# Kernel tuning notes

Measured on AMD Instinct MI355X. Metric: run time of the kernel, lower is better.

## Reference

```python
import jax, jax.numpy as jnp
import numpy as np

B, C, Hs, Ws = 8, 512, 32, 32
NUM_HEADS, D_K = 8, 64
SCALE = D_K ** -0.5


def setup_inputs() -> dict:
    key = jax.random.key(0)
    ks = jax.random.split(key, 8)
    inner = NUM_HEADS * D_K  # 512
    s = 0.02
    return {
        "x": jax.random.normal(ks[0], (B, C, Hs, Ws), dtype=jnp.float32),
        "y": jax.random.normal(ks[1], (B, C, Hs, Ws), dtype=jnp.float32),
        "Wq": jax.random.normal(ks[2], (inner, C), dtype=jnp.float32) * s,
        "bq": jnp.zeros((inner,), dtype=jnp.float32),
        "Wkv": jax.random.normal(ks[3], (2 * inner, C), dtype=jnp.float32) * s,
        "bkv": jnp.zeros((2 * inner,), dtype=jnp.float32),
        "Wp": jax.random.normal(ks[4], (C, inner), dtype=jnp.float32) * s,
        "bp": jnp.zeros((C,), dtype=jnp.float32),
    }


def reference(x, y, Wq, bq, Wkv, bkv, Wp, bp):
    # Faithful to CrossAttentionBlock.forward: y is only shape-checked, unused.
    x_shape = x.shape
    b, c = x.shape[0], x.shape[1]
    # channel_transfer: [B, C, H, W] -> [B, H, W, C] -> [B, N, C]
    xt = jnp.transpose(x, (0, 2, 3, 1)).reshape(b, -1, c)
    n = xt.shape[1]
    # q: [B, N, H*dk] -> [B, H, N, dk]
    q = (xt @ Wq.T + bq).reshape(b, n, NUM_HEADS, D_K).transpose(0, 2, 1, 3)
    # kv: [B, N, 2*H*dk] -> [2, B, H, N, dk]
    kv = (xt @ Wkv.T + bkv).reshape(b, n, 2, NUM_HEADS, D_K).transpose(2, 0, 3, 1, 4)
    k, v = kv[0], kv[1]
    atten = jnp.einsum("bhik,bhjk->bhij", q, k) * SCALE
    atten = jax.nn.softmax(atten, axis=-1)
    res = jnp.einsum("bhij,bhjd->bhid", atten, v)  # [B, H, N, dk]
    res = res.transpose(0, 2, 1, 3).reshape(b, n, NUM_HEADS * D_K)
    res = res @ Wp.T + bp  # [B, N, C]
    # original does a raw reshape of [B, N, C] back into x_shape [B, C, H, W]
    return res.reshape(x_shape)
```

## Files before the change

### kernel.cpp

```cpp
#include <hip/hip_runtime.h>
#include <math.h>

#define BB 8
#define CC 512
#define NH 8
#define DK 64
#define NN 1024
#define MROWS (BB * NN)
#define INNER 512
#define SCALE 0.125f


typedef __attribute__((ext_vector_type(8))) short bf16x8;
typedef __attribute__((ext_vector_type(4))) float floatx4;

__device__ inline short f2bf(float f) {
    union { float f; unsigned u; } un;
    un.f = f;
    unsigned r = un.u + 0x7fffu + ((un.u >> 16) & 1u);
    return (short)(r >> 16);
}

__device__ inline short f2bf_rhu(float f) {
    union { float f; unsigned u; } un;
    un.f = f;
    return (short)((un.u + 0x8000u) >> 16);
}

#define GLD_LDS(gptr, lptr)                                                  \
    __builtin_amdgcn_global_load_lds(                                        \
        (const __attribute__((address_space(1))) void*)(gptr),               \
        (__attribute__((address_space(3))) void*)(lptr), 16, 0, 0)

__global__ __launch_bounds__(256) void prep_kernel(
    const float* __restrict__ x, const float* __restrict__ Wq,
    const float* __restrict__ Wkv, const float* __restrict__ Wp,
    const float* __restrict__ bq, const float* __restrict__ bkv,
    short* __restrict__ xtb, short* __restrict__ wqkvb,
    short* __restrict__ wpb, float* __restrict__ bqkv) {
    __shared__ float tile[32][33];
    const int bid = blockIdx.x;
    if (bid < 4096) {
        const int n0 = (bid & 31) * 32;
        const int c0 = ((bid >> 5) & 15) * 32;
        const int b = bid >> 9;
        const int tx = threadIdx.x & 31;
        const int ty = threadIdx.x >> 5;
        const float* xb = x + (size_t)b * CC * NN;
        short* xo = xtb + (size_t)b * NN * CC;
        for (int i = ty; i < 32; i += 8)
            tile[i][tx] = xb[(size_t)(c0 + i) * NN + n0 + tx];
        __syncthreads();
        for (int i = ty; i < 32; i += 8)
            xo[(size_t)(n0 + i) * CC + c0 + tx] = f2bf(tile[tx][i]);
    } else {
        const int i = (bid - 4096) * 1024 + threadIdx.x * 4;
        if (i < 786432) {
            float4 v = (i < 262144) ? *(const float4*)&Wq[i]
                                    : *(const float4*)&Wkv[i - 262144];
            wqkvb[i + 0] = f2bf(v.x);
            wqkvb[i + 1] = f2bf(v.y);
            wqkvb[i + 2] = f2bf(v.z);
            wqkvb[i + 3] = f2bf(v.w);
        } else if (i < 1048576) {
            const int j = i - 786432;
            float4 v = *(const float4*)&Wp[j];
            wpb[j + 0] = f2bf(v.x);
            wpb[j + 1] = f2bf(v.y);
            wpb[j + 2] = f2bf(v.z);
            wpb[j + 3] = f2bf(v.w);
        } else {
            const int j = i - 1048576;
            if (j < 1536) {
                float4 v = (j < 512) ? *(const float4*)&bq[j]
                                     : *(const float4*)&bkv[j - 512];
                *(float4*)&bqkv[j] = v;
            }
        }
    }
}

template <int MODE, int BN>
__global__ __launch_bounds__(256) void gemm_mfma_kernel(
    const short* __restrict__ A, const short* __restrict__ W,
    const float* __restrict__ bias, float* __restrict__ outf,
    short* __restrict__ outq, short* __restrict__ outk,
    short* __restrict__ outv) {
    constexpr int K = 512;
    constexpr int WCOLS = BN / 64;
    constexpr int WROWS = 4 / WCOLS;
    constexpr int WRSPAN = 128 / WROWS;
    constexpr int RT = WRSPAN / 16;
    constexpr int ABUF = 128 * 32;
    constexpr int BBUF = BN * 32;
    constexpr int STAGE_EL = 2 * ABUF + 2 * BBUF;
    constexpr int CS_EL = (MODE == 1) ? 128 * 132 : 0;
    constexpr int SMEM_EL = (CS_EL > STAGE_EL) ? CS_EL : STAGE_EL;
    __shared__ short smem[SMEM_EL];
    short* As = smem;
    short* Bs = smem + 2 * ABUF;

    const int t = threadIdx.x;
    const int wave = t >> 6;
    const int lane = t & 63;
    const int col = lane & 15;
    const int quad = lane >> 4;
    const int wr = wave / WCOLS;
    const int wc = wave % WCOLS;

    const int bm0 = blockIdx.x * 128;
    const int bn0 = blockIdx.y * BN;

    floatx4 acc[RT][4];
#pragma unroll
    for (int i = 0; i < RT; i++)
#pragma unroll
        for (int j = 0; j < 4; j++) acc[i][j] = (floatx4){0.f, 0.f, 0.f, 0.f};

    const int kpE = (lane & 3) * 8;
    const int rA = wave * 32 + (lane >> 2);
    const short* Ag = A + (size_t)(bm0 + rA) * K + kpE;
    const int rB = wave * (BN / 4) + (lane >> 2);
    const short* Wg = W + (size_t)(bn0 + rB) * K + kpE;
    const int aOff = wave * 1024;
    const int bOff = wave * (BN / 4) * 32;

#define GSTAGE(K0, BUF)                                                       \
    do {                                                                      \
        GLD_LDS(Ag + (K0), As + (BUF)*ABUF + aOff);                           \
        GLD_LDS(Ag + 16 * K + (K0), As + (BUF)*ABUF + aOff + 512);            \
        if constexpr (BN == 128) {                                            \
            GLD_LDS(Wg + (K0), Bs + (BUF)*BBUF + bOff);                       \
            GLD_LDS(Wg + 16 * K + (K0), Bs + (BUF)*BBUF + bOff + 512);        \
        } else {                                                              \
            GLD_LDS(Wg + (K0), Bs + (BUF)*BBUF + bOff);                       \
        }                                                                     \
    } while (0)

    GSTAGE(0, 0);

#pragma unroll
    for (int it = 0; it < 16; it++) {
        const int buf = it & 1;
        __syncthreads();
        if (it < 15) GSTAGE((it + 1) * 32, buf ^ 1);

        const short* A_ = As + buf * ABUF;
        const short* B_ = Bs + buf * BBUF;
        bf16x8 aF[RT], bF[4];
#pragma unroll
        for (int rt = 0; rt < RT; rt++)
            aF[rt] =
                *(const bf16x8*)&A_[(wr * WRSPAN + rt * 16 + col) * 32 + quad * 8];
#pragma unroll
        for (int ct = 0; ct < 4; ct++)
            bF[ct] = *(const bf16x8*)&B_[(wc * 64 + ct * 16 + col) * 32 + quad * 8];
#pragma unroll
        for (int rt = 0; rt < RT; rt++)
#pragma unroll
            for (int ct = 0; ct < 4; ct++)
                acc[rt][ct] = __builtin_amdgcn_mfma_f32_16x16x32_bf16(
                    aF[rt], bF[ct], acc[rt][ct], 0, 0, 0);
    }
#undef GSTAGE

    if (MODE == 1) {
        short* Cs = smem;
        const bool isV = (bn0 >= 1024);
        const bool isQ = (bn0 < 512);
        __syncthreads();
        if (isV) {
#pragma unroll
            for (int rt = 0; rt < RT; rt++) {
#pragma unroll
                for (int ct = 0; ct < 4; ct++) {
                    const int jn_l = wc * 64 + ct * 16 + col;
                    const float bsv = bias[bn0 + jn_l];
                    const int m_l = wr * WRSPAN + rt * 16 + quad * 4;
                    short4 v4;
                    v4.x = f2bf(acc[rt][ct][0] + bsv);
                    v4.y = f2bf(acc[rt][ct][1] + bsv);
                    v4.z = f2bf(acc[rt][ct][2] + bsv);
                    v4.w = f2bf(acc[rt][ct][3] + bsv);
                    *(short4*)&Cs[jn_l * 132 + m_l] = v4;
                }
            }
        } else {
#pragma unroll
            for (int rt = 0; rt < RT; rt++) {
#pragma unroll
                for (int ct = 0; ct < 4; ct++) {
                    const int jn_l = wc * 64 + ct * 16 + col;
                    const float bsv = bias[bn0 + jn_l];
#pragma unroll
                    for (int r = 0; r < 4; r++) {
                        const int m_l = wr * WRSPAN + rt * 16 + quad * 4 + r;
                        const float val = acc[rt][ct][r] + bsv;
                        Cs[m_l * 132 + jn_l] =
                            isQ ? f2bf(val * SCALE) : f2bf(val);
                    }
                }
            }
        }
        __syncthreads();
        const int b = bm0 >> 10;
        const int nbase = bm0 & 1023;
        if (isV) {
#pragma unroll
            for (int p = 0; p < 8; p++) {
                const int cid = p * 256 + t;
                const int jn_l = cid >> 4;
                const int m0 = (cid & 15) * 8;
                bf16x8 frag = *(const bf16x8*)&Cs[jn_l * 132 + m0];
                const int jn_g = bn0 + jn_l;
                const int h = (jn_g >> 6) & 7;
                const int d = jn_g & 63;
                *(bf16x8*)&outv[(((size_t)(b * NH + h)) * DK + d) * NN + nbase +
                                m0] = frag;
            }
        } else {
            short* dst = isQ ? outq : outk;
#pragma unroll
            for (int p = 0; p < 8; p++) {
                const int cid = p * 256 + t;
                const int m_l = cid >> 4;
                const int jn0 = (cid & 15) * 8;
                bf16x8 frag = *(const bf16x8*)&Cs[m_l * 132 + jn0];
                const int jn_g = bn0 + jn0;
                const int h = (jn_g >> 6) & 7;
                const int d = jn_g & 63;
                *(bf16x8*)&dst[(((size_t)(b * NH + h)) * NN + nbase + m_l) * DK +
                               d] = frag;
            }
        }
        return;
    }

#pragma unroll
    for (int rt = 0; rt < RT; rt++) {
#pragma unroll
        for (int ct = 0; ct < 4; ct++) {
            const int jn = bn0 + wc * 64 + ct * 16 + col;
            const float bsv = bias[jn];
#pragma unroll
            for (int r = 0; r < 4; r++) {
                const int m = bm0 + wr * WRSPAN + rt * 16 + quad * 4 + r;
                outf[(size_t)m * 512 + jn] = acc[rt][ct][r] + bsv;
            }
        }
    }
}

__global__ __launch_bounds__(512) void attn_mfma_kernel(
    const short* __restrict__ q, const short* __restrict__ k,
    const short* __restrict__ vt, short* __restrict__ out) {
    const int bh = blockIdx.x;
    const int b = bh >> 3;
    const int h = bh & 7;
    const int n0 = blockIdx.y * 128;
    const int tid = threadIdx.x;
    const int wave = tid >> 6;
    const int lane = tid & 63;
    const int col = lane & 15;
    const int quad = lane >> 4;

    __shared__ short Ks[2][64 * 64];
    __shared__ short Vs[2][64 * 64];
    __shared__ short Ps[8][16][72];

    bf16x8 qa0, qa1;
    {
        const size_t qoff = ((size_t)bh * NN + n0 + wave * 16 + col) * DK;
        qa0 = *(const bf16x8*)&q[qoff + quad * 8];
        qa1 = *(const bf16x8*)&q[qoff + 32 + quad * 8];
    }

    floatx4 o[4];
#pragma unroll
    for (int i = 0; i < 4; i++) o[i] = (floatx4){0.f, 0.f, 0.f, 0.f};
    float l_run[4] = {0.f, 0.f, 0.f, 0.f};

    const short* kg = k + (size_t)bh * NN * DK;
    const short* vg = vt + (size_t)bh * DK * NN;

    const int srow = lane >> 3;
    const int sunit = (lane & 7) ^ srow;
    const int sbase = (wave & 3) * 16;

    const int xs = col & 7;
    const int pK0 = (quad ^ xs) * 8;
    const int pK1 = ((quad + 4) ^ xs) * 8;

#define STAGE(J0, BUF)                                                         \
    do {                                                                       \
        if (wave < 4) {                                                        \
            GLD_LDS(kg + (size_t)((J0) + sbase + srow) * DK + sunit * 8,       \
                    &Ks[BUF][sbase * 64]);                                     \
            GLD_LDS(kg + (size_t)((J0) + sbase + 8 + srow) * DK + sunit * 8,   \
                    &Ks[BUF][(sbase + 8) * 64]);                               \
        } else {                                                               \
            GLD_LDS(vg + (size_t)(sbase + srow) * NN + (J0) + sunit * 8,       \
                    &Vs[BUF][sbase * 64]);                                     \
            GLD_LDS(vg + (size_t)(sbase + 8 + srow) * NN + (J0) + sunit * 8,   \
                    &Vs[BUF][(sbase + 8) * 64]);                               \
        }                                                                      \
    } while (0)

    STAGE(0, 0);

    for (int c = 0; c < 16; c++) {
        const int buf = c & 1;
        __syncthreads();
        if (c < 15) STAGE((c + 1) * 64, buf ^ 1);

        const short* K_ = &Ks[buf][0];
        const short* V_ = &Vs[buf][0];

        float p[4][4];
#pragma unroll
        for (int ct = 0; ct < 4; ct++) {
            bf16x8 kb0 = *(const bf16x8*)&K_[(ct * 16 + col) * 64 + pK0];
            bf16x8 kb1 = *(const bf16x8*)&K_[(ct * 16 + col) * 64 + pK1];
            floatx4 acc = (floatx4){0.f, 0.f, 0.f, 0.f};
            acc = __builtin_amdgcn_mfma_f32_16x16x32_bf16(qa0, kb0, acc, 0, 0, 0);
            acc = __builtin_amdgcn_mfma_f32_16x16x32_bf16(qa1, kb1, acc, 0, 0, 0);
#pragma unroll
            for (int r = 0; r < 4; r++) p[ct][r] = __expf(acc[r]);
        }

#pragma unroll
        for (int r = 0; r < 4; r++)
            l_run[r] += (p[0][r] + p[1][r]) + (p[2][r] + p[3][r]);

#pragma unroll
        for (int ct = 0; ct < 4; ct++)
#pragma unroll
            for (int r = 0; r < 4; r++)
                Ps[wave][quad * 4 + r][ct * 16 + col] = f2bf_rhu(p[ct][r]);

        bf16x8 pa0 = *(const bf16x8*)&Ps[wave][col][quad * 8];
        bf16x8 pa1 = *(const bf16x8*)&Ps[wave][col][32 + quad * 8];

#pragma unroll
        for (int dt = 0; dt < 4; dt++) {
            bf16x8 vb0 = *(const bf16x8*)&V_[(dt * 16 + col) * 64 + pK0];
            bf16x8 vb1 = *(const bf16x8*)&V_[(dt * 16 + col) * 64 + pK1];
            o[dt] = __builtin_amdgcn_mfma_f32_16x16x32_bf16(pa0, vb0, o[dt], 0, 0, 0);
            o[dt] = __builtin_amdgcn_mfma_f32_16x16x32_bf16(pa1, vb1, o[dt], 0, 0, 0);
        }
    }
#undef STAGE

    float inv[4];
#pragma unroll
    for (int r = 0; r < 4; r++) {
        float lv = l_run[r];
#pragma unroll
        for (int d = 1; d < 16; d <<= 1) lv += __shfl_xor(lv, d, 64);
        inv[r] = 1.f / lv;
    }
#pragma unroll
    for (int dt = 0; dt < 4; dt++)
#pragma unroll
        for (int r = 0; r < 4; r++)
            Ps[wave][quad * 4 + r][dt * 16 + col] = f2bf(o[dt][r] * inv[r]);

    {
        const int row = lane >> 2;
        const int d0 = (lane & 3) * 16;
        bf16x8 f0 = *(const bf16x8*)&Ps[wave][row][d0];
        bf16x8 f1 = *(const bf16x8*)&Ps[wave][row][d0 + 8];
        const int m = n0 + wave * 16 + row;
        short* orow = out + ((size_t)(b * NN + m)) * 512 + h * 64 + d0;
        *(bf16x8*)&orow[0] = f0;
        *(bf16x8*)&orow[8] = f1;
    }
}

extern "C" void kernel_launch(void* const* d_in, const int* in_sizes, int n_in,
                              void* d_out, int out_size, void* d_ws,
                              size_t ws_size, hipStream_t stream) {
    const float* x = (const float*)d_in[0];
    const float* Wq = (const float*)d_in[2];
    const float* bq = (const float*)d_in[3];
    const float* Wkv = (const float*)d_in[4];
    const float* bkv = (const float*)d_in[5];
    const float* Wp = (const float*)d_in[6];
    const float* bp = (const float*)d_in[7];
    float* out = (float*)d_out;

    short* ws = (short*)d_ws;
    short* xtb = ws;
    short* qb = xtb + (size_t)MROWS * CC;
    short* kb = qb + (size_t)MROWS * INNER;
    short* vb = kb + (size_t)MROWS * INNER;
    short* wqkvb = vb + (size_t)MROWS * INNER;
    short* wpb = wqkvb + (size_t)3 * INNER * CC;
    float* bqkv = (float*)(wpb + (size_t)CC * INNER);
    short* att = xtb;

    prep_kernel<<<4096 + 1026, 256, 0, stream>>>(x, Wq, Wkv, Wp, bq, bkv, xtb,
                                                 wqkvb, wpb, bqkv);
    {
        dim3 grid(MROWS / 128, (3 * INNER) / 128);
        gemm_mfma_kernel<1, 128><<<grid, 256, 0, stream>>>(
            xtb, wqkvb, bqkv, nullptr, qb, kb, vb);
    }
    {
        dim3 grid(BB * NH, NN / 128);
        attn_mfma_kernel<<<grid, 512, 0, stream>>>(qb, kb, vb, att);
    }
    {
        dim3 grid(MROWS / 128, CC / 64);
        gemm_mfma_kernel<0, 64><<<grid, 256, 0, stream>>>(
            att, wpb, bp, out, nullptr, nullptr, nullptr);
    }
}
```

Baseline: 150.9 us.

## Process two query row tiles per wave in attention kernel, halving block size

Each wave now handles 32 query rows (two 16-row MFMA tiles) instead of 16, so each K and V fragment read from LDS feeds two MFMAs. Blocks shrink from 512 to 256 threads, and every wave stages both K and V. The aim is to halve LDS fragment traffic per unit of MFMA work. In exchange, register pressure per wave roughly doubles for accumulators and probabilities, and each block has fewer waves to hide latency.

```diff
diff --git a/kernel.cpp b/kernel.cpp
--- a/kernel.cpp
+++ b/kernel.cpp
@@ -251,7 +251,7 @@
     }
 }
 
-__global__ __launch_bounds__(512) void attn_mfma_kernel(
+__global__ __launch_bounds__(256) void attn_mfma_kernel(
     const short* __restrict__ q, const short* __restrict__ k,
     const short* __restrict__ vt, short* __restrict__ out) {
     const int bh = blockIdx.x;
@@ -266,26 +266,30 @@
 
     __shared__ short Ks[2][64 * 64];
     __shared__ short Vs[2][64 * 64];
-    __shared__ short Ps[8][16][72];
-
-    bf16x8 qa0, qa1;
-    {
-        const size_t qoff = ((size_t)bh * NN + n0 + wave * 16 + col) * DK;
-        qa0 = *(const bf16x8*)&q[qoff + quad * 8];
-        qa1 = *(const bf16x8*)&q[qoff + 32 + quad * 8];
-    }
-
-    floatx4 o[4];
-#pragma unroll
-    for (int i = 0; i < 4; i++) o[i] = (floatx4){0.f, 0.f, 0.f, 0.f};
-    float l_run[4] = {0.f, 0.f, 0.f, 0.f};
+    __shared__ short Ps[4][32][72];
+
+    bf16x8 qa[2][2];
+#pragma unroll
+    for (int rt = 0; rt < 2; rt++) {
+        const size_t qoff =
+            ((size_t)bh * NN + n0 + wave * 32 + rt * 16 + col) * DK;
+        qa[rt][0] = *(const bf16x8*)&q[qoff + quad * 8];
+        qa[rt][1] = *(const bf16x8*)&q[qoff + 32 + quad * 8];
+    }
+
+    floatx4 o[2][4];
+#pragma unroll
+    for (int rt = 0; rt < 2; rt++)
+#pragma unroll
+        for (int i = 0; i < 4; i++) o[rt][i] = (floatx4){0.f, 0.f, 0.f, 0.f};
+    float l_run[2][4] = {{0.f, 0.f, 0.f, 0.f}, {0.f, 0.f, 0.f, 0.f}};
 
     const short* kg = k + (size_t)bh * NN * DK;
     const short* vg = vt + (size_t)bh * DK * NN;
 
     const int srow = lane >> 3;
     const int sunit = (lane & 7) ^ srow;
-    const int sbase = (wave & 3) * 16;
+    const int sbase = wave * 16;
 
     const int xs = col & 7;
     const int pK0 = (quad ^ xs) * 8;
@@ -293,17 +297,14 @@
 
 #define STAGE(J0, BUF)                                                         \
     do {                                                                       \
-        if (wave < 4) {                                                        \
-            GLD_LDS(kg + (size_t)((J0) + sbase + srow) * DK + sunit * 8,       \
-                    &Ks[BUF][sbase * 64]);                                     \
-            GLD_LDS(kg + (size_t)((J0) + sbase + 8 + srow) * DK + sunit * 8,   \
-                    &Ks[BUF][(sbase + 8) * 64]);                               \
-        } else {                                                               \
-            GLD_LDS(vg + (size_t)(sbase + srow) * NN + (J0) + sunit * 8,       \
-                    &Vs[BUF][sbase * 64]);                                     \
-            GLD_LDS(vg + (size_t)(sbase + 8 + srow) * NN + (J0) + sunit * 8,   \
-                    &Vs[BUF][(sbase + 8) * 64]);                               \
-        }                                                                      \
+        GLD_LDS(kg + (size_t)((J0) + sbase + srow) * DK + sunit * 8,           \
+                &Ks[BUF][sbase * 64]);                                         \
+        GLD_LDS(kg + (size_t)((J0) + sbase + 8 + srow) * DK + sunit * 8,       \
+                &Ks[BUF][(sbase + 8) * 64]);                                   \
+        GLD_LDS(vg + (size_t)(sbase + srow) * NN + (J0) + sunit * 8,           \
+                &Vs[BUF][sbase * 64]);                                         \
+        GLD_LDS(vg + (size_t)(sbase + 8 + srow) * NN + (J0) + sunit * 8,       \
+                &Vs[BUF][(sbase + 8) * 64]);                                   \
     } while (0)
 
     STAGE(0, 0);
@@ -316,61 +317,87 @@
         const short* K_ = &Ks[buf][0];
         const short* V_ = &Vs[buf][0];
 
-        float p[4][4];
+        float p[2][4][4];
 #pragma unroll
         for (int ct = 0; ct < 4; ct++) {
             bf16x8 kb0 = *(const bf16x8*)&K_[(ct * 16 + col) * 64 + pK0];
             bf16x8 kb1 = *(const bf16x8*)&K_[(ct * 16 + col) * 64 + pK1];
-            floatx4 acc = (floatx4){0.f, 0.f, 0.f, 0.f};
-            acc = __builtin_amdgcn_mfma_f32_16x16x32_bf16(qa0, kb0, acc, 0, 0, 0);
-            acc = __builtin_amdgcn_mfma_f32_16x16x32_bf16(qa1, kb1, acc, 0, 0, 0);
-#pragma unroll
-            for (int r = 0; r < 4; r++) p[ct][r] = __expf(acc[r]);
-        }
-
-#pragma unroll
-        for (int r = 0; r < 4; r++)
-            l_run[r] += (p[0][r] + p[1][r]) + (p[2][r] + p[3][r]);
-
-#pragma unroll
-        for (int ct = 0; ct < 4; ct++)
+#pragma unroll
+            for (int rt = 0; rt < 2; rt++) {
+                floatx4 acc = (floatx4){0.f, 0.f, 0.f, 0.f};
+                acc = __builtin_amdgcn_mfma_f32_16x16x32_bf16(qa[rt][0], kb0,
+                                                              acc, 0, 0, 0);
+                acc = __builtin_amdgcn_mfma_f32_16x16x32_bf16(qa[rt][1], kb1,
+                                                              acc, 0, 0, 0);
+#pragma unroll
+                for (int r = 0; r < 4; r++) p[rt][ct][r] = __expf(acc[r]);
+            }
+        }
+
+#pragma unroll
+        for (int rt = 0; rt < 2; rt++)
 #pragma unroll
             for (int r = 0; r < 4; r++)
-                Ps[wave][quad * 4 + r][ct * 16 + col] = f2bf_rhu(p[ct][r]);
-
-        bf16x8 pa0 = *(const bf16x8*)&Ps[wave][col][quad * 8];
-        bf16x8 pa1 = *(const bf16x8*)&Ps[wave][col][32 + quad * 8];
+                l_run[rt][r] +=
+                    (p[rt][0][r] + p[rt][1][r]) + (p[rt][2][r] + p[rt][3][r]);
+
+#pragma unroll
+        for (int rt = 0; rt < 2; rt++)
+#pragma unroll
+            for (int ct = 0; ct < 4; ct++)
+#pragma unroll
+                for (int r = 0; r < 4; r++)
+                    Ps[wave][rt * 16 + quad * 4 + r][ct * 16 + col] =
+                        f2bf_rhu(p[rt][ct][r]);
+
+        bf16x8 pa[2][2];
+#pragma unroll
+        for (int rt = 0; rt < 2; rt++) {
+            pa[rt][0] = *(const bf16x8*)&Ps[wave][rt * 16 + col][quad * 8];
+            pa[rt][1] = *(const bf16x8*)&Ps[wave][rt * 16 + col][32 + quad * 8];
+        }
 
 #pragma unroll
         for (int dt = 0; dt < 4; dt++) {
             bf16x8 vb0 = *(const bf16x8*)&V_[(dt * 16 + col) * 64 + pK0];
             bf16x8 vb1 = *(const bf16x8*)&V_[(dt * 16 + col) * 64 + pK1];
-            o[dt] = __builtin_amdgcn_mfma_f32_16x16x32_bf16(pa0, vb0, o[dt], 0, 0, 0);
-            o[dt] = __builtin_amdgcn_mfma_f32_16x16x32_bf16(pa1, vb1, o[dt], 0, 0, 0);
+#pragma unroll
+            for (int rt = 0; rt < 2; rt++) {
+                o[rt][dt] = __builtin_amdgcn_mfma_f32_16x16x32_bf16(
+                    pa[rt][0], vb0, o[rt][dt], 0, 0, 0);
+                o[rt][dt] = __builtin_amdgcn_mfma_f32_16x16x32_bf16(
+                    pa[rt][1], vb1, o[rt][dt], 0, 0, 0);
+            }
         }
     }
 #undef STAGE
 
-    float inv[4];
-#pragma unroll
-    for (int r = 0; r < 4; r++) {
-        float lv = l_run[r];
-#pragma unroll
-        for (int d = 1; d < 16; d <<= 1) lv += __shfl_xor(lv, d, 64);
-        inv[r] = 1.f / lv;
-    }
-#pragma unroll
-    for (int dt = 0; dt < 4; dt++)
-#pragma unroll
-        for (int r = 0; r < 4; r++)
-            Ps[wave][quad * 4 + r][dt * 16 + col] = f2bf(o[dt][r] * inv[r]);
-
-    {
+    float inv[2][4];
+#pragma unroll
+    for (int rt = 0; rt < 2; rt++)
+#pragma unroll
+        for (int r = 0; r < 4; r++) {
+            float lv = l_run[rt][r];
+#pragma unroll
+            for (int d = 1; d < 16; d <<= 1) lv += __shfl_xor(lv, d, 64);
+            inv[rt][r] = 1.f / lv;
+        }
+#pragma unroll
+    for (int rt = 0; rt < 2; rt++)
+#pragma unroll
+        for (int dt = 0; dt < 4; dt++)
+#pragma unroll
+            for (int r = 0; r < 4; r++)
+                Ps[wave][rt * 16 + quad * 4 + r][dt * 16 + col] =
+                    f2bf(o[rt][dt][r] * inv[rt][r]);
+
+#pragma unroll
+    for (int rt = 0; rt < 2; rt++) {
         const int row = lane >> 2;
         const int d0 = (lane & 3) * 16;
-        bf16x8 f0 = *(const bf16x8*)&Ps[wave][row][d0];
-        bf16x8 f1 = *(const bf16x8*)&Ps[wave][row][d0 + 8];
-        const int m = n0 + wave * 16 + row;
+        bf16x8 f0 = *(const bf16x8*)&Ps[wave][rt * 16 + row][d0];
+        bf16x8 f1 = *(const bf16x8*)&Ps[wave][rt * 16 + row][d0 + 8];
+        const int m = n0 + wave * 32 + rt * 16 + row;
         short* orow = out + ((size_t)(b * NN + m)) * 512 + h * 64 + d0;
         *(bf16x8*)&orow[0] = f0;
         *(bf16x8*)&orow[8] = f1;
@@ -408,7 +435,7 @@
     }
     {
         dim3 grid(BB * NH, NN / 128);
-        attn_mfma_kernel<<<grid, 512, 0, stream>>>(qb, kb, vb, att);
+        attn_mfma_kernel<<<grid, 256, 0, stream>>>(qb, kb, vb, att);
     }
     {
         dim3 grid(MROWS / 128, CC / 64);
```

New measurement: 152.1 us. Within noise of the previous version (+0.8%).
